# Kernel optimization log

Hardware: AMD Instinct MI355X
Metric: run time of the kernel (lower is better)

The kernel has to match this reference:

```python
import jax, jax.numpy as jnp
import numpy as np

TEMPERATURE = 0.5
SCALE_LOSS = 1.0 / 32.0
LAMBDA = 0.0039


def setup_inputs() -> dict:
    key = jax.random.key(0)
    z = jax.random.normal(key, (4096, 6, 256), dtype=jnp.float32)
    return {"z": z}


def reference(z):
    B, V = z.shape[0], z.shape[1]
    # [B, V, ...] -> [V, B, D], L2-normalize embeddings
    zv = z.reshape(B, V, -1).transpose(1, 0, 2)
    zn = zv / jnp.linalg.norm(zv, axis=-1, keepdims=True)

    # Positive error: per-sample cross-view similarity [B, V, V]
    sim_pos = jnp.einsum('vbd,wbd->bvw', zn, zn)
    pos = jnp.exp((1.0 - sim_pos) / TEMPERATURE).mean(axis=(1, 2))  # [B]

    # Negative error: per-view within-batch similarity [V, B, B]
    sim_neg = jnp.exp(jnp.einsum('vbd,vcd->vbc', zn, zn) / TEMPERATURE)
    offdiag_mask = ~jnp.eye(B, dtype=bool)  # [B, B]
    off_mean = jnp.where(offdiag_mask[None], sim_neg, 0.0).sum(-1) / (B - 1)  # [V, B]
    neg = off_mean.sum(0)  # [B], accumulated over views

    return jnp.sum(pos) * SCALE_LOSS + LAMBDA * jnp.sum(neg)
```

## Files before the change

kernel.cpp:

```cpp
#include <hip/hip_runtime.h>
#include <cstdint>
#include <cstddef>

#define B_N 4096
#define V_N 6
#define D_N 256
#define NTILE 528
#define NBLK (NTILE * V_N)

typedef int i32x4 __attribute__((ext_vector_type(4)));

#define QC 298.0f
#define INV_C2_X2 (2.0f / (QC * QC))

__device__ __forceinline__ void async_load16(void* lds, const void* gmem) {
  __builtin_amdgcn_global_load_lds(
      (const __attribute__((address_space(1))) unsigned int*)gmem,
      (__attribute__((address_space(3))) unsigned int*)lds,
      16, 0, 0);
}

__global__ __launch_bounds__(256) void norm_pos_kernel(
    const float* __restrict__ z, signed char* __restrict__ znb,
    float* __restrict__ pos_part) {
  const int b = blockIdx.x;
  const int t = threadIdx.x;
  const int lane = t & 63;
  const int w = t >> 6;

  __shared__ float zs[V_N][D_N];
  __shared__ float red[V_N][4];
  __shared__ float inv[V_N];
  __shared__ float pred[4];

  const float* zb = z + (size_t)b * (V_N * D_N);
#pragma unroll
  for (int v = 0; v < V_N; ++v) zs[v][t] = zb[v * D_N + t];
  __syncthreads();

#pragma unroll
  for (int v = 0; v < V_N; ++v) {
    float x = zs[v][t];
    float s = x * x;
#pragma unroll
    for (int off = 32; off > 0; off >>= 1) s += __shfl_down(s, off);
    if (lane == 0) red[v][w] = s;
  }
  __syncthreads();
  if (t < V_N) inv[t] = rsqrtf(red[t][0] + red[t][1] + red[t][2] + red[t][3]);
  __syncthreads();

#pragma unroll
  for (int v = 0; v < V_N; ++v) {
    float q = rintf(zs[v][t] * inv[v] * QC);
    q = fminf(127.0f, fmaxf(-127.0f, q));
    znb[((size_t)v * B_N + b) * D_N + t] = (signed char)(int)q;
  }

  float psum = 0.0f;
  int pidx = 0;
#pragma unroll
  for (int v = 0; v < V_N; ++v) {
#pragma unroll
    for (int u = v + 1; u < V_N; ++u) {
      if ((pidx & 3) == w) {
        float s = 0.0f;
#pragma unroll
        for (int d = 0; d < D_N; d += 64) s += zs[v][lane + d] * zs[u][lane + d];
#pragma unroll
        for (int off = 32; off > 0; off >>= 1) s += __shfl_down(s, off);
        if (lane == 0) {
          float sim = s * inv[v] * inv[u];
          psum += __expf(2.0f * (1.0f - sim));
        }
      }
      ++pidx;
    }
  }
  if (lane == 0) pred[w] = psum;
  __syncthreads();
  if (t == 0) pos_part[b] = pred[0] + pred[1] + pred[2] + pred[3];
}

__global__ __launch_bounds__(256) void gram_kernel(
    const signed char* __restrict__ znb, float* __restrict__ neg_part) {
  const int v = blockIdx.y;
  const int t = blockIdx.x;
  int i = (int)((sqrtf(8.0f * (float)t + 1.0f) - 1.0f) * 0.5f);
  while ((i + 1) * (i + 2) / 2 <= t) ++i;
  while (i * (i + 1) / 2 > t) --i;
  const int j = t - i * (i + 1) / 2;

  const signed char* Zv = znb + (size_t)v * B_N * D_N;
  const signed char* Ag = Zv + (size_t)(i * 128) * D_N;
  const signed char* Bg = Zv + (size_t)(j * 128) * D_N;

  __shared__ signed char As[128][64];
  __shared__ signed char Bs[128][64];
  __shared__ float blk[4];

  const int tid = threadIdx.x;
  const int lane = tid & 63;
  const int w = tid >> 6;
  const int wr = w >> 1;
  const int wc = w & 1;

  i32x4 c[4][4];
#pragma unroll
  for (int a = 0; a < 4; ++a)
#pragma unroll
    for (int b2 = 0; b2 < 4; ++b2) c[a][b2] = (i32x4){0, 0, 0, 0};

  const int kc = lane >> 4;
  const int mrow = wr * 64 + (lane & 15);
  const int ncol = wc * 64 + (lane & 15);

  signed char* AsF = &As[0][0];
  signed char* BsF = &Bs[0][0];

  for (int k0 = 0; k0 < D_N; k0 += 64) {
    __syncthreads();
#pragma unroll
    for (int q = 0; q < 2; ++q) {
      const int s = tid + 256 * q;
      const int row = s >> 2;
      const int gc = (s & 3) ^ (row & 3) ^ ((row >> 2) & 3);
      async_load16(AsF + s * 16, Ag + (size_t)row * D_N + k0 + gc * 16);
      async_load16(BsF + s * 16, Bg + (size_t)row * D_N + k0 + gc * 16);
    }
    __syncthreads();

    i32x4 af[4], bfr[4];
#pragma unroll
    for (int f = 0; f < 4; ++f) {
      const int ra = mrow + 16 * f;
      const int rb2 = ncol + 16 * f;
      const int ca = kc ^ (ra & 3) ^ ((ra >> 2) & 3);
      const int cb2 = kc ^ (rb2 & 3) ^ ((rb2 >> 2) & 3);
      af[f]  = *(const i32x4*)(AsF + ra * 64 + ca * 16);
      bfr[f] = *(const i32x4*)(BsF + rb2 * 64 + cb2 * 16);
    }
#pragma unroll
    for (int fm = 0; fm < 4; ++fm)
#pragma unroll
      for (int fn = 0; fn < 4; ++fn)
        c[fm][fn] = __builtin_amdgcn_mfma_i32_16x16x64_i8(
            af[fm], bfr[fn], c[fm][fn], 0, 0, 0);
  }

  float lsum = 0.0f;
  const int rb = i * 128 + wr * 64 + (lane >> 4) * 4;
  const int cb = j * 128 + wc * 64 + (lane & 15);
#pragma unroll
  for (int fm = 0; fm < 4; ++fm) {
#pragma unroll
    for (int fn = 0; fn < 4; ++fn) {
      const int gcol = cb + fn * 16;
#pragma unroll
      for (int r = 0; r < 4; ++r) {
        const int grow = rb + fm * 16 + r;
        float e = __expf((float)c[fm][fn][r] * INV_C2_X2);
        lsum += (grow == gcol) ? 0.0f : e;
      }
    }
  }
  if (i != j) lsum *= 2.0f;

#pragma unroll
  for (int off = 32; off > 0; off >>= 1) lsum += __shfl_down(lsum, off);
  if (lane == 0) blk[w] = lsum;
  __syncthreads();
  if (tid == 0) neg_part[t + NTILE * v] = blk[0] + blk[1] + blk[2] + blk[3];
}

__global__ __launch_bounds__(1024) void finalize_kernel(
    const float* __restrict__ pos_part, const float* __restrict__ neg_part,
    float* __restrict__ out) {
  const int t = threadIdx.x;
  const int lane = t & 63;
  const int w = t >> 6;
  __shared__ float pr[16], nr[16];

  float p = 0.0f;
  for (int idx = t; idx < B_N; idx += 1024) p += pos_part[idx];
  float n = 0.0f;
  for (int idx = t; idx < NBLK; idx += 1024) n += neg_part[idx];
#pragma unroll
  for (int off = 32; off > 0; off >>= 1) {
    p += __shfl_down(p, off);
    n += __shfl_down(n, off);
  }
  if (lane == 0) { pr[w] = p; nr[w] = n; }
  __syncthreads();
  if (t == 0) {
    float P = 0.0f, N = 0.0f;
#pragma unroll
    for (int k = 0; k < 16; ++k) { P += pr[k]; N += nr[k]; }
    out[0] = (1.0f / 32.0f) * ((float)B_N / 6.0f + P / 18.0f) +
             0.0039f * (N / (float)(B_N - 1));
  }
}

extern "C" void kernel_launch(void* const* d_in, const int* in_sizes, int n_in,
                              void* d_out, int out_size, void* d_ws, size_t ws_size,
                              hipStream_t stream) {
  const float* z = (const float*)d_in[0];
  float* out = (float*)d_out;
  float* pos_part = (float*)d_ws;
  float* neg_part = (float*)((char*)d_ws + 16384);
  signed char* znb = (signed char*)((char*)d_ws + 32768);

  norm_pos_kernel<<<B_N, 256, 0, stream>>>(z, znb, pos_part);
  dim3 grid(NTILE, V_N, 1);
  gram_kernel<<<grid, 256, 0, stream>>>(znb, neg_part);
  finalize_kernel<<<1, 1024, 0, stream>>>(pos_part, neg_part, out);
}
```

Baseline: 110.3 us.

## Load Gram MFMA fragments directly from global memory, vectorize z load

The int8 Gram kernel no longer stages A/B tiles through LDS with async global_load_lds and two barriers per K step. Each lane now reads its 16-byte MFMA fragments straight from global memory (relying on L1/L2 caching), and the K loop is fully unrolled. The normalization kernel also loads z as float4 instead of scalar floats. This removes LDS traffic and barriers, but duplicates global reads across waves sharing rows and may expose more memory latency.

New measurement: 132.9 us. 20.5% more time.

```diff
diff --git a/kernel.cpp b/kernel.cpp
--- a/kernel.cpp
+++ b/kernel.cpp
@@ -13,13 +13,6 @@
 #define QC 298.0f
 #define INV_C2_X2 (2.0f / (QC * QC))
 
-__device__ __forceinline__ void async_load16(void* lds, const void* gmem) {
-  __builtin_amdgcn_global_load_lds(
-      (const __attribute__((address_space(1))) unsigned int*)gmem,
-      (__attribute__((address_space(3))) unsigned int*)lds,
-      16, 0, 0);
-}
-
 __global__ __launch_bounds__(256) void norm_pos_kernel(
     const float* __restrict__ z, signed char* __restrict__ znb,
     float* __restrict__ pos_part) {
@@ -33,9 +26,10 @@
   __shared__ float inv[V_N];
   __shared__ float pred[4];
 
-  const float* zb = z + (size_t)b * (V_N * D_N);
-#pragma unroll
-  for (int v = 0; v < V_N; ++v) zs[v][t] = zb[v * D_N + t];
+  const float4* zb4 = (const float4*)(z + (size_t)b * (V_N * D_N));
+  float4* zs4 = (float4*)&zs[0][0];
+  zs4[t] = zb4[t];
+  if (t < 384 - 256) zs4[256 + t] = zb4[256 + t];
   __syncthreads();
 
 #pragma unroll
@@ -92,11 +86,7 @@
   const int j = t - i * (i + 1) / 2;
 
   const signed char* Zv = znb + (size_t)v * B_N * D_N;
-  const signed char* Ag = Zv + (size_t)(i * 128) * D_N;
-  const signed char* Bg = Zv + (size_t)(j * 128) * D_N;
 
-  __shared__ signed char As[128][64];
-  __shared__ signed char Bs[128][64];
   __shared__ float blk[4];
 
   const int tid = threadIdx.x;
@@ -105,40 +95,26 @@
   const int wr = w >> 1;
   const int wc = w & 1;
 
+  const int kc = lane >> 4;
+  const int mrow = wr * 64 + (lane & 15);
+  const int ncol = wc * 64 + (lane & 15);
+
+  const signed char* Ab = Zv + (size_t)(i * 128 + mrow) * D_N + kc * 16;
+  const signed char* Bb = Zv + (size_t)(j * 128 + ncol) * D_N + kc * 16;
+
   i32x4 c[4][4];
 #pragma unroll
   for (int a = 0; a < 4; ++a)
 #pragma unroll
     for (int b2 = 0; b2 < 4; ++b2) c[a][b2] = (i32x4){0, 0, 0, 0};
 
-  const int kc = lane >> 4;
-  const int mrow = wr * 64 + (lane & 15);
-  const int ncol = wc * 64 + (lane & 15);
-
-  signed char* AsF = &As[0][0];
-  signed char* BsF = &Bs[0][0];
-
+#pragma unroll
   for (int k0 = 0; k0 < D_N; k0 += 64) {
-    __syncthreads();
-#pragma unroll
-    for (int q = 0; q < 2; ++q) {
-      const int s = tid + 256 * q;
-      const int row = s >> 2;
-      const int gc = (s & 3) ^ (row & 3) ^ ((row >> 2) & 3);
-      async_load16(AsF + s * 16, Ag + (size_t)row * D_N + k0 + gc * 16);
-      async_load16(BsF + s * 16, Bg + (size_t)row * D_N + k0 + gc * 16);
-    }
-    __syncthreads();
-
     i32x4 af[4], bfr[4];
 #pragma unroll
     for (int f = 0; f < 4; ++f) {
-      const int ra = mrow + 16 * f;
-      const int rb2 = ncol + 16 * f;
-      const int ca = kc ^ (ra & 3) ^ ((ra >> 2) & 3);
-      const int cb2 = kc ^ (rb2 & 3) ^ ((rb2 >> 2) & 3);
-      af[f]  = *(const i32x4*)(AsF + ra * 64 + ca * 16);
-      bfr[f] = *(const i32x4*)(BsF + rb2 * 64 + cb2 * 16);
+      af[f]  = *(const i32x4*)(Ab + (size_t)f * 16 * D_N + k0);
+      bfr[f] = *(const i32x4*)(Bb + (size_t)f * 16 * D_N + k0);
     }
 #pragma unroll
     for (int fm = 0; fm < 4; ++fm)
```
